# Optimization experiments

Hardware: AMD Instinct MI355X
Metric: run time of the kernel (lower is better)

## Reference

```python
import jax, jax.numpy as jnp
import numpy as np

NUM_ITERS = 3
EPS_ATTN = 1e-8
LN_EPS = 1e-3  # tf.keras LayerNormalization default epsilon


def layernorm(x, g, b):
    m = jnp.mean(x, axis=-1, keepdims=True)
    v = jnp.var(x, axis=-1, keepdims=True)
    return (x - m) * jax.lax.rsqrt(v + LN_EPS) * g + b


def setup_inputs() -> dict:
    key = jax.random.key(0)
    ks = jax.random.split(key, 20)
    B, N, Din, S, D, H = 64, 4096, 64, 7, 64, 128

    def glorot(k, shape):
        fan_in, fan_out = shape[-2], shape[-1]
        lim = np.sqrt(6.0 / (fan_in + fan_out))
        return jax.random.uniform(k, shape, jnp.float32, -lim, lim)

    return {
        "inputs": jax.random.normal(ks[0], (B, N, Din), jnp.float32),
        "slot_noise": jax.random.normal(ks[1], (B, S, D), jnp.float32),
        "ln_in_g": jnp.ones((Din,), jnp.float32), "ln_in_b": jnp.zeros((Din,), jnp.float32),
        "ln_s_g": jnp.ones((D,), jnp.float32), "ln_s_b": jnp.zeros((D,), jnp.float32),
        "ln_m_g": jnp.ones((D,), jnp.float32), "ln_m_b": jnp.zeros((D,), jnp.float32),
        "Wq": glorot(ks[2], (D, D)),
        "Wk": glorot(ks[3], (Din, D)),
        "Wv": glorot(ks[4], (Din, D)),
        "slots_mu": glorot(ks[5], (1, 1, D)),
        "slots_log_sigma": glorot(ks[6], (1, 1, D)),
        "gru_W": glorot(ks[7], (D, 3 * D)),
        "gru_U": glorot(ks[8], (D, 3 * D)),
        "gru_b": jnp.zeros((2, 3 * D), jnp.float32),  # [input_bias, recurrent_bias] (reset_after=True)
        "W1": glorot(ks[9], (D, H)), "b1": jnp.zeros((H,), jnp.float32),
        "W2": glorot(ks[10], (H, D)), "b2": jnp.zeros((D,), jnp.float32),
    }


def reference(inputs, slot_noise, ln_in_g, ln_in_b, ln_s_g, ln_s_b, ln_m_g, ln_m_b,
              Wq, Wk, Wv, slots_mu, slots_log_sigma, gru_W, gru_U, gru_b,
              W1, b1, W2, b2):
    D = Wq.shape[0]
    x = layernorm(inputs, ln_in_g, ln_in_b)          # [B,N,Din]
    k = x @ Wk                                       # [B,N,D]
    v = x @ Wv                                       # [B,N,D]
    slots = slots_mu + jnp.exp(slots_log_sigma) * slot_noise  # [B,S,D]

    scale = D ** (-0.5)
    for _ in range(NUM_ITERS):
        slots_prev = slots
        s = layernorm(slots, ln_s_g, ln_s_b)
        q = (s @ Wq) * scale                         # [B,S,D]
        logits = jnp.einsum("bnd,bsd->bns", k, q)   # [B,N,S]
        attn = jax.nn.softmax(logits, axis=-1) + EPS_ATTN
        attn = attn / jnp.sum(attn, axis=-2, keepdims=True)  # normalize over inputs N
        updates = jnp.einsum("bns,bnd->bsd", attn, v)        # [B,S,D]
        # GRUCell (Keras v2: reset_after=True, sigmoid recurrent activation)
        mx = updates @ gru_W + gru_b[0]
        mh = slots_prev @ gru_U + gru_b[1]
        xz, xr, xh = jnp.split(mx, 3, axis=-1)
        hz, hr, hh = jnp.split(mh, 3, axis=-1)
        z = jax.nn.sigmoid(xz + hz)
        r = jax.nn.sigmoid(xr + hr)
        hcand = jnp.tanh(xh + r * hh)
        slots = z * slots_prev + (1.0 - z) * hcand
        # MLP with residual
        m = layernorm(slots, ln_m_g, ln_m_b)
        slots = slots + jax.nn.relu(m @ W1 + b1) @ W2 + b2
    return slots
```

## Files before the change

### kernel.cpp

```cpp
#include <hip/hip_runtime.h>
#include <hip/hip_bf16.h>


#define NB 64
#define NN 4096
#define NS 7
#define LN_EPS 1e-3f
#define EPS_ATTN 1e-8f

typedef __attribute__((ext_vector_type(8))) __bf16 bf16x8;
typedef __attribute__((ext_vector_type(8))) unsigned short u16x8;
typedef __attribute__((ext_vector_type(4))) float f32x4;
typedef __attribute__((ext_vector_type(4))) unsigned int u32x4;

__device__ __forceinline__ unsigned short f2bf(float f) {
    unsigned int x = __float_as_uint(f);
    x += 0x7FFFu + ((x >> 16) & 1u);
    return (unsigned short)(x >> 16);
}

__device__ __forceinline__ bf16x8 pack8(float4 a, float4 b) {
    u16x8 r;
    r[0] = f2bf(a.x); r[1] = f2bf(a.y); r[2] = f2bf(a.z); r[3] = f2bf(a.w);
    r[4] = f2bf(b.x); r[5] = f2bf(b.y); r[6] = f2bf(b.z); r[7] = f2bf(b.w);
    return __builtin_bit_cast(bf16x8, r);
}

__global__ __launch_bounds__(64) void prep_kernel(
        const float* __restrict__ Wk, const float* __restrict__ Wv,
        const float* __restrict__ g, const float* __restrict__ bb,
        unsigned short* __restrict__ GkT, unsigned short* __restrict__ GvT,
        float* __restrict__ cgk, float* __restrict__ cbk,
        float* __restrict__ cgv, float* __restrict__ cbv) {
    int j = blockIdx.x & 63, mat = blockIdx.x >> 6, d = threadIdx.x;
    const float* W = mat ? Wv : Wk;
    unsigned short* GT = mat ? GvT : GkT;
    float* cg = mat ? cgv : cgk;
    float* cb = mat ? cbv : cbk;
    float w = W[d * 64 + j];
    float gv = g[d], bv = bb[d];
    GT[j * 64 + d] = f2bf(gv * w);
    float sg = gv * w, sb = bv * w;
#pragma unroll
    for (int off = 1; off < 64; off <<= 1) {
        sg += __shfl_xor(sg, off);
        sb += __shfl_xor(sb, off);
    }
    if (d == 0) { cg[j] = sg; cb[j] = sb; }
}

__global__ void init_slots_kernel(const float* __restrict__ noise, const float* __restrict__ mu,
                                  const float* __restrict__ lsig, float* __restrict__ slots) {
    int idx = blockIdx.x * 256 + threadIdx.x;
    if (idx < NB * NS * 64) {
        int d = idx & 63;
        slots[idx] = mu[d] + __expf(lsig[d]) * noise[idx];
    }
}

__global__ __launch_bounds__(256) void proj_kernel(
        const float* __restrict__ x, const unsigned short* __restrict__ GkT,
        const unsigned short* __restrict__ GvT,
        const float* __restrict__ cgk, const float* __restrict__ cbk,
        const float* __restrict__ cgv, const float* __restrict__ cbv,
        unsigned short* __restrict__ kout, unsigned short* __restrict__ vT) {
    int t = threadIdx.x;
    int w = t >> 6, lane = t & 63;
    int h = lane >> 4, rl = lane & 15;
    long base = (long)blockIdx.x * 128;
    int bb = blockIdx.x >> 5;
    int nblk = (blockIdx.x & 31) * 128;
    const float* xr0 = x + (base + w * 16 + rl) * 64 + h * 8;
    const float* xr1 = xr0 + 64 * 64;
    float4 xa[8];
    xa[0] = *(const float4*)(xr0);      xa[1] = *(const float4*)(xr0 + 4);
    xa[2] = *(const float4*)(xr0 + 32); xa[3] = *(const float4*)(xr0 + 36);
    xa[4] = *(const float4*)(xr1);      xa[5] = *(const float4*)(xr1 + 4);
    xa[6] = *(const float4*)(xr1 + 32); xa[7] = *(const float4*)(xr1 + 36);
    float s1a = 0.f, s2a = 0.f, s1b = 0.f, s2b = 0.f;
#pragma unroll
    for (int i = 0; i < 4; ++i) {
        s1a += xa[i].x + xa[i].y + xa[i].z + xa[i].w;
        s2a += xa[i].x * xa[i].x + xa[i].y * xa[i].y + xa[i].z * xa[i].z + xa[i].w * xa[i].w;
        s1b += xa[4 + i].x + xa[4 + i].y + xa[4 + i].z + xa[4 + i].w;
        s2b += xa[4 + i].x * xa[4 + i].x + xa[4 + i].y * xa[4 + i].y + xa[4 + i].z * xa[4 + i].z + xa[4 + i].w * xa[4 + i].w;
    }
    s1a += __shfl_xor(s1a, 16); s2a += __shfl_xor(s2a, 16);
    s1a += __shfl_xor(s1a, 32); s2a += __shfl_xor(s2a, 32);
    s1b += __shfl_xor(s1b, 16); s2b += __shfl_xor(s2b, 16);
    s1b += __shfl_xor(s1b, 32); s2b += __shfl_xor(s2b, 32);
    float m0 = s1a * (1.f / 64.f);
    float i0 = rsqrtf(s2a * (1.f / 64.f) - m0 * m0 + LN_EPS);
    float m1 = s1b * (1.f / 64.f);
    float i1 = rsqrtf(s2b * (1.f / 64.f) - m1 * m1 + LN_EPS);
    bf16x8 a00 = pack8(xa[0], xa[1]), a01 = pack8(xa[2], xa[3]);
    bf16x8 a10 = pack8(xa[4], xa[5]), a11 = pack8(xa[6], xa[7]);
    f32x4 k0a[4], v0a[4], k1a[4], v1a[4];
#pragma unroll
    for (int nt = 0; nt < 4; ++nt) {
        k0a[nt] = (f32x4){0.f, 0.f, 0.f, 0.f}; v0a[nt] = (f32x4){0.f, 0.f, 0.f, 0.f};
        k1a[nt] = (f32x4){0.f, 0.f, 0.f, 0.f}; v1a[nt] = (f32x4){0.f, 0.f, 0.f, 0.f};
    }
#pragma unroll
    for (int nt = 0; nt < 4; ++nt) {
        const unsigned short* gk = GkT + (nt * 16 + rl) * 64 + h * 8;
        const unsigned short* gv = GvT + (nt * 16 + rl) * 64 + h * 8;
        bf16x8 bk0 = *(const bf16x8*)(gk);
        bf16x8 bk1 = *(const bf16x8*)(gk + 32);
        bf16x8 bv0 = *(const bf16x8*)(gv);
        bf16x8 bv1 = *(const bf16x8*)(gv + 32);
        k0a[nt] = __builtin_amdgcn_mfma_f32_16x16x32_bf16(a00, bk0, k0a[nt], 0, 0, 0);
        k0a[nt] = __builtin_amdgcn_mfma_f32_16x16x32_bf16(a01, bk1, k0a[nt], 0, 0, 0);
        v0a[nt] = __builtin_amdgcn_mfma_f32_16x16x32_bf16(a00, bv0, v0a[nt], 0, 0, 0);
        v0a[nt] = __builtin_amdgcn_mfma_f32_16x16x32_bf16(a01, bv1, v0a[nt], 0, 0, 0);
        k1a[nt] = __builtin_amdgcn_mfma_f32_16x16x32_bf16(a10, bk0, k1a[nt], 0, 0, 0);
        k1a[nt] = __builtin_amdgcn_mfma_f32_16x16x32_bf16(a11, bk1, k1a[nt], 0, 0, 0);
        v1a[nt] = __builtin_amdgcn_mfma_f32_16x16x32_bf16(a10, bv0, v1a[nt], 0, 0, 0);
        v1a[nt] = __builtin_amdgcn_mfma_f32_16x16x32_bf16(a11, bv1, v1a[nt], 0, 0, 0);
    }
    float mr0[4], ir0[4], mr1[4], ir1[4];
#pragma unroll
    for (int r = 0; r < 4; ++r) {
        int rlsrc = h * 4 + r;
        mr0[r] = __shfl(m0, rlsrc); ir0[r] = __shfl(i0, rlsrc);
        mr1[r] = __shfl(m1, rlsrc); ir1[r] = __shfl(i1, rlsrc);
    }
#pragma unroll
    for (int nt = 0; nt < 4; ++nt) {
        int j = nt * 16 + rl;
        float cgkj = cgk[j], cbkj = cbk[j], cgvj = cgv[j], cbvj = cbv[j];
        unsigned int vp0 = 0, vp1 = 0;
#pragma unroll
        for (int r = 0; r < 4; ++r) {
            long row = base + w * 16 + h * 4 + r;
            kout[row * 64 + j] = f2bf(ir0[r] * (k0a[nt][r] - mr0[r] * cgkj) + cbkj);
            unsigned int vb = f2bf(ir0[r] * (v0a[nt][r] - mr0[r] * cgvj) + cbvj);
            if (r < 2) vp0 |= vb << (16 * r); else vp1 |= vb << (16 * (r - 2));
        }
        {
            long vaddr = ((long)(bb * 64 + j)) * NN + nblk + w * 16 + h * 4;
            *(uint2*)(vT + vaddr) = make_uint2(vp0, vp1);
        }
        vp0 = 0; vp1 = 0;
#pragma unroll
        for (int r = 0; r < 4; ++r) {
            long row = base + 64 + w * 16 + h * 4 + r;
            kout[row * 64 + j] = f2bf(ir1[r] * (k1a[nt][r] - mr1[r] * cgkj) + cbkj);
            unsigned int vb = f2bf(ir1[r] * (v1a[nt][r] - mr1[r] * cgvj) + cbvj);
            if (r < 2) vp0 |= vb << (16 * r); else vp1 |= vb << (16 * (r - 2));
        }
        {
            long vaddr = ((long)(bb * 64 + j)) * NN + nblk + 64 + w * 16 + h * 4;
            *(uint2*)(vT + vaddr) = make_uint2(vp0, vp1);
        }
    }
}

__global__ __launch_bounds__(64) void slots_pre_kernel(
        const float* __restrict__ slots, const float* __restrict__ Wq,
        const float* __restrict__ lg, const float* __restrict__ lb,
        float* __restrict__ q, float* __restrict__ U, float* __restrict__ Z) {
    __shared__ float sn[64];
    int bs = blockIdx.x, d = threadIdx.x;
    float xv = slots[bs * 64 + d];
    float s1 = xv, s2 = xv * xv;
#pragma unroll
    for (int off = 1; off < 64; off <<= 1) {
        s1 += __shfl_xor(s1, off);
        s2 += __shfl_xor(s2, off);
    }
    float m = s1 * (1.f / 64.f);
    float inv = rsqrtf(s2 * (1.f / 64.f) - m * m + LN_EPS);
    sn[d] = (xv - m) * inv * lg[d] + lb[d];
    __syncthreads();
    float acc = 0.f;
#pragma unroll 8
    for (int i = 0; i < 64; ++i) acc += sn[i] * Wq[i * 64 + d];
    q[bs * 64 + d] = acc * 0.125f;
    U[bs * 64 + d] = 0.f;
    if (d == 0) Z[bs] = 0.f;
}

__global__ __launch_bounds__(256) void attn_kernel(
        const unsigned short* __restrict__ kp, const unsigned short* __restrict__ vtp,
        const float* __restrict__ q, float* __restrict__ U, float* __restrict__ Z) {
    __shared__ unsigned int plds[4][320];
    __shared__ float ured[4][512];
    int t = threadIdx.x;
    int b = blockIdx.x >> 4, blk = blockIdx.x & 15;
    int w = t >> 6, lane = t & 63;
    int h = lane >> 4, c = lane & 15;
    bf16x8 qf0, qf1;
    {
        int cs = (c < 7) ? c : 0;
        const float* qr = q + (b * NS + cs) * 64 + h * 8;
        float4 q0 = *(const float4*)(qr);
        float4 q1 = *(const float4*)(qr + 4);
        float4 q2 = *(const float4*)(qr + 32);
        float4 q3 = *(const float4*)(qr + 36);
        if (c >= 7) {
            q0 = make_float4(0.f, 0.f, 0.f, 0.f); q1 = q0; q2 = q0; q3 = q0;
        }
        qf0 = pack8(q0, q1);
        qf1 = pack8(q2, q3);
    }
    f32x4 pv[4];
#pragma unroll
    for (int i = 0; i < 4; ++i) pv[i] = (f32x4){0.f, 0.f, 0.f, 0.f};
    float zac = 0.f;
    unsigned int* pw = plds[w];
    long rb0 = (long)b * NN + blk * 256 + w * 16;
#pragma unroll
    for (int p = 0; p < 2; ++p) {
#pragma unroll
        for (int sh = 0; sh < 2; ++sh) {
            long rowbase = rb0 + p * 128 + sh * 64;
            const unsigned short* ka = kp + (rowbase + c) * 64 + h * 8;
            bf16x8 a0 = *(const bf16x8*)(ka);
            bf16x8 a1 = *(const bf16x8*)(ka + 32);
            f32x4 lg = (f32x4){0.f, 0.f, 0.f, 0.f};
            lg = __builtin_amdgcn_mfma_f32_16x16x32_bf16(a0, qf0, lg, 0, 0, 0);
            lg = __builtin_amdgcn_mfma_f32_16x16x32_bf16(a1, qf1, lg, 0, 0, 0);
            float av[4];
#pragma unroll
            for (int j = 0; j < 4; ++j) {
                float vl = (c < 7) ? lg[j] : -1e30f;
                float mx = vl;
                mx = fmaxf(mx, __shfl_xor(mx, 1));
                mx = fmaxf(mx, __shfl_xor(mx, 2));
                mx = fmaxf(mx, __shfl_xor(mx, 4));
                mx = fmaxf(mx, __shfl_xor(mx, 8));
                float e = (c < 7) ? __expf(lg[j] - mx) : 0.f;
                float se = e;
                se += __shfl_xor(se, 1);
                se += __shfl_xor(se, 2);
                se += __shfl_xor(se, 4);
                se += __shfl_xor(se, 8);
                float a = (c < 7) ? (__fdividef(e, se) + EPS_ATTN) : 0.f;
                av[j] = a;
                zac += a;
            }
            unsigned int w0 = (unsigned int)f2bf(av[0]) | ((unsigned int)f2bf(av[1]) << 16);
            unsigned int w1 = (unsigned int)f2bf(av[2]) | ((unsigned int)f2bf(av[3]) << 16);
            pw[c * 20 + sh * 8 + 2 * h]     = w0;
            pw[c * 20 + sh * 8 + 2 * h + 1] = w1;
        }
        u32x4 pr = *(u32x4*)(&pw[c * 20 + 4 * h]);
        bf16x8 pa = __builtin_bit_cast(bf16x8, pr);
        int nb = blk * 256 + p * 128 + ((h < 2) ? (w * 16 + 8 * h) : (48 + w * 16 + 8 * h));
#pragma unroll
        for (int tile = 0; tile < 4; ++tile) {
            const unsigned short* vb = vtp + ((long)(b * 64 + tile * 16 + c)) * NN + nb;
            bf16x8 bv = *(const bf16x8*)(vb);
            pv[tile] = __builtin_amdgcn_mfma_f32_16x16x32_bf16(pa, bv, pv[tile], 0, 0, 0);
        }
    }
    zac += __shfl_xor(zac, 16);
    zac += __shfl_xor(zac, 32);
    if (h == 0 && c < 7) atomicAdd(Z + b * NS + c, zac);
    if (h < 2) {
#pragma unroll
        for (int tile = 0; tile < 4; ++tile) {
#pragma unroll
            for (int j = 0; j < 4; ++j) {
                ured[w][(4 * h + j) * 64 + tile * 16 + c] = pv[tile][j];
            }
        }
    }
    __syncthreads();
    for (int idx = t; idx < NS * 64; idx += 256) {
        float tot = ured[0][idx] + ured[1][idx] + ured[2][idx] + ured[3][idx];
        atomicAdd(U + b * NS * 64 + idx, tot);
    }
}

__global__ __launch_bounds__(256) void slots_post_kernel(
        float* __restrict__ slots, float* __restrict__ U, float* __restrict__ Z,
        const float* __restrict__ gW, const float* __restrict__ gU, const float* __restrict__ gb,
        const float* __restrict__ lmg, const float* __restrict__ lmb,
        const float* __restrict__ W1, const float* __restrict__ b1,
        const float* __restrict__ W2, const float* __restrict__ b2,
        const float* __restrict__ Wq, const float* __restrict__ lsg, const float* __restrict__ lsb,
        float* __restrict__ q, float* __restrict__ outp, int last) {
    __shared__ float up[64], hp[64], mx[192], mh[192], mm[64], hl[128], sn[64];
    int bs = blockIdx.x, t = threadIdx.x;
    if (t < 64) {
        float zsum = Z[bs];
        up[t] = U[bs * 64 + t] / zsum;
        hp[t] = slots[bs * 64 + t];
        U[bs * 64 + t] = 0.f;
        if (t == 0) Z[bs] = 0.f;
    }
    __syncthreads();
    if (t < 192) {
        float xa0 = gb[t], ha0 = gb[192 + t], xa1 = 0.f, ha1 = 0.f;
#pragma unroll 8
        for (int i = 0; i < 64; i += 2) {
            xa0 += up[i] * gW[i * 192 + t];
            ha0 += hp[i] * gU[i * 192 + t];
            xa1 += up[i + 1] * gW[(i + 1) * 192 + t];
            ha1 += hp[i + 1] * gU[(i + 1) * 192 + t];
        }
        mx[t] = xa0 + xa1; mh[t] = ha0 + ha1;
    }
    __syncthreads();
    float hnew = 0.f;
    if (t < 64) {
        float z = 1.f / (1.f + __expf(-(mx[t] + mh[t])));
        float r = 1.f / (1.f + __expf(-(mx[64 + t] + mh[64 + t])));
        float pre = mx[128 + t] + r * mh[128 + t];
        pre = fminf(fmaxf(pre, -15.f), 15.f);
        float e2 = __expf(2.f * pre);
        float hc = (e2 - 1.f) / (e2 + 1.f);
        hnew = z * hp[t] + (1.f - z) * hc;
        float s1 = hnew, s2 = hnew * hnew;
#pragma unroll
        for (int off = 1; off < 64; off <<= 1) { s1 += __shfl_xor(s1, off); s2 += __shfl_xor(s2, off); }
        float m = s1 * (1.f / 64.f);
        float inv = rsqrtf(s2 * (1.f / 64.f) - m * m + LN_EPS);
        mm[t] = (hnew - m) * inv * lmg[t] + lmb[t];
    }
    __syncthreads();
    if (t < 128) {
        float h1 = b1[t], h2 = 0.f;
#pragma unroll 8
        for (int i = 0; i < 64; i += 2) {
            h1 += mm[i] * W1[i * 128 + t];
            h2 += mm[i + 1] * W1[(i + 1) * 128 + t];
        }
        hl[t] = fmaxf(h1 + h2, 0.f);
    }
    __syncthreads();
    if (t < 64) {
        float o = hnew + b2[t], o1 = 0.f;
#pragma unroll 8
        for (int j = 0; j < 128; j += 2) {
            o += hl[j] * W2[j * 64 + t];
            o1 += hl[j + 1] * W2[(j + 1) * 64 + t];
        }
        o += o1;
        slots[bs * 64 + t] = o;
        if (last) outp[bs * 64 + t] = o;
        float s1 = o, s2 = o * o;
#pragma unroll
        for (int off = 1; off < 64; off <<= 1) { s1 += __shfl_xor(s1, off); s2 += __shfl_xor(s2, off); }
        float m = s1 * (1.f / 64.f);
        float inv = rsqrtf(s2 * (1.f / 64.f) - m * m + LN_EPS);
        sn[t] = (o - m) * inv * lsg[t] + lsb[t];
    }
    __syncthreads();
    if (t < 64) {
        float acc = 0.f;
#pragma unroll 8
        for (int i = 0; i < 64; ++i) acc += sn[i] * Wq[i * 64 + t];
        q[bs * 64 + t] = acc * 0.125f;
    }
}

extern "C" void kernel_launch(void* const* d_in, const int* in_sizes, int n_in,
                              void* d_out, int out_size, void* d_ws, size_t ws_size,
                              hipStream_t stream) {
    const float* inputs  = (const float*)d_in[0];
    const float* noise   = (const float*)d_in[1];
    const float* ln_in_g = (const float*)d_in[2];
    const float* ln_in_b = (const float*)d_in[3];
    const float* ln_s_g  = (const float*)d_in[4];
    const float* ln_s_b  = (const float*)d_in[5];
    const float* ln_m_g  = (const float*)d_in[6];
    const float* ln_m_b  = (const float*)d_in[7];
    const float* Wq      = (const float*)d_in[8];
    const float* Wk      = (const float*)d_in[9];
    const float* Wv      = (const float*)d_in[10];
    const float* mu      = (const float*)d_in[11];
    const float* lsig    = (const float*)d_in[12];
    const float* gW      = (const float*)d_in[13];
    const float* gU      = (const float*)d_in[14];
    const float* gb      = (const float*)d_in[15];
    const float* W1      = (const float*)d_in[16];
    const float* b1      = (const float*)d_in[17];
    const float* W2      = (const float*)d_in[18];
    const float* b2      = (const float*)d_in[19];

    char* ws = (char*)d_ws;
    unsigned short* kbuf = (unsigned short*)ws;
    unsigned short* vtbuf = (unsigned short*)(ws + 33554432);
    float* slots = (float*)(ws + 67108864);
    float* qbuf  = (float*)(ws + 67108864 + 114688);
    float* Ubuf  = (float*)(ws + 67108864 + 2 * 114688);
    float* Zbuf  = (float*)(ws + 67108864 + 3 * 114688);
    unsigned short* GkT = (unsigned short*)(ws + 67108864 + 3 * 114688 + 4096);
    unsigned short* GvT = GkT + 4096;
    float* cgk = (float*)(GvT + 4096);
    float* cbk = cgk + 64;
    float* cgv = cbk + 64;
    float* cbv = cgv + 64;

    prep_kernel<<<128, 64, 0, stream>>>(Wk, Wv, ln_in_g, ln_in_b, GkT, GvT, cgk, cbk, cgv, cbv);
    init_slots_kernel<<<112, 256, 0, stream>>>(noise, mu, lsig, slots);
    proj_kernel<<<2048, 256, 0, stream>>>(inputs, GkT, GvT, cgk, cbk, cgv, cbv, kbuf, vtbuf);
    slots_pre_kernel<<<448, 64, 0, stream>>>(slots, Wq, ln_s_g, ln_s_b, qbuf, Ubuf, Zbuf);
    for (int it = 0; it < 3; ++it) {
        attn_kernel<<<1024, 256, 0, stream>>>(kbuf, vtbuf, qbuf, Ubuf, Zbuf);
        slots_post_kernel<<<448, 256, 0, stream>>>(slots, Ubuf, Zbuf, gW, gU, gb,
                                                   ln_m_g, ln_m_b, W1, b1, W2, b2,
                                                   Wq, ln_s_g, ln_s_b, qbuf,
                                                   (float*)d_out, (it == 2) ? 1 : 0);
    }
}
```

Before: 256.5 us.

## Stage K/V tiles through LDS for coalesced stores and fuse slot init into projection

The projection kernel now writes its K and transposed V outputs into padded LDS tiles and then emits fully coalesced 16-byte global stores. Slot initialization and the slot pre-processing (layernorm, Q projection, U/Z zeroing) are folded into the first 448 blocks of that kernel, removing two launches. The attention kernel preloads all K fragments into registers and copies its V^T tile into LDS up front instead of issuing scattered global loads inside the loop. The cost is much higher LDS use per block, which may reduce occupancy, plus extra barriers.

Result: no change. 253.1 us (-1.3%).

```diff
diff --git a/kernel.cpp b/kernel.cpp
--- a/kernel.cpp
+++ b/kernel.cpp
@@ -49,21 +49,20 @@
     if (d == 0) { cg[j] = sg; cb[j] = sb; }
 }
 
-__global__ void init_slots_kernel(const float* __restrict__ noise, const float* __restrict__ mu,
-                                  const float* __restrict__ lsig, float* __restrict__ slots) {
-    int idx = blockIdx.x * 256 + threadIdx.x;
-    if (idx < NB * NS * 64) {
-        int d = idx & 63;
-        slots[idx] = mu[d] + __expf(lsig[d]) * noise[idx];
-    }
-}
-
 __global__ __launch_bounds__(256) void proj_kernel(
         const float* __restrict__ x, const unsigned short* __restrict__ GkT,
         const unsigned short* __restrict__ GvT,
         const float* __restrict__ cgk, const float* __restrict__ cbk,
         const float* __restrict__ cgv, const float* __restrict__ cbv,
-        unsigned short* __restrict__ kout, unsigned short* __restrict__ vT) {
+        unsigned short* __restrict__ kout, unsigned short* __restrict__ vT,
+        const float* __restrict__ noise, const float* __restrict__ mu,
+        const float* __restrict__ lsig,
+        const float* __restrict__ Wq, const float* __restrict__ lsg,
+        const float* __restrict__ lsb,
+        float* __restrict__ slots, float* __restrict__ q,
+        float* __restrict__ U, float* __restrict__ Z) {
+    __shared__ __align__(16) unsigned short ktile[128 * 72];
+    __shared__ __align__(16) unsigned short vtile[64 * 136];
     int t = threadIdx.x;
     int w = t >> 6, lane = t & 63;
     int h = lane >> 4, rl = lane & 15;
@@ -83,7 +82,8 @@
         s1a += xa[i].x + xa[i].y + xa[i].z + xa[i].w;
         s2a += xa[i].x * xa[i].x + xa[i].y * xa[i].y + xa[i].z * xa[i].z + xa[i].w * xa[i].w;
         s1b += xa[4 + i].x + xa[4 + i].y + xa[4 + i].z + xa[4 + i].w;
-        s2b += xa[4 + i].x * xa[4 + i].x + xa[4 + i].y * xa[4 + i].y + xa[4 + i].z * xa[4 + i].z + xa[4 + i].w * xa[4 + i].w;
+        s2b += xa[4 + i].x * xa[4 + i].x + xa[4 + i].y * xa[4 + i].y
+             + xa[4 + i].z * xa[4 + i].z + xa[4 + i].w * xa[4 + i].w;
     }
     s1a += __shfl_xor(s1a, 16); s2a += __shfl_xor(s2a, 16);
     s1a += __shfl_xor(s1a, 32); s2a += __shfl_xor(s2a, 32);
@@ -129,67 +129,87 @@
     for (int nt = 0; nt < 4; ++nt) {
         int j = nt * 16 + rl;
         float cgkj = cgk[j], cbkj = cbk[j], cgvj = cgv[j], cbvj = cbv[j];
-        unsigned int vp0 = 0, vp1 = 0;
+        unsigned short vv0[4], vv1[4];
 #pragma unroll
         for (int r = 0; r < 4; ++r) {
-            long row = base + w * 16 + h * 4 + r;
-            kout[row * 64 + j] = f2bf(ir0[r] * (k0a[nt][r] - mr0[r] * cgkj) + cbkj);
-            unsigned int vb = f2bf(ir0[r] * (v0a[nt][r] - mr0[r] * cgvj) + cbvj);
-            if (r < 2) vp0 |= vb << (16 * r); else vp1 |= vb << (16 * (r - 2));
-        }
-        {
-            long vaddr = ((long)(bb * 64 + j)) * NN + nblk + w * 16 + h * 4;
-            *(uint2*)(vT + vaddr) = make_uint2(vp0, vp1);
-        }
-        vp0 = 0; vp1 = 0;
-#pragma unroll
-        for (int r = 0; r < 4; ++r) {
-            long row = base + 64 + w * 16 + h * 4 + r;
-            kout[row * 64 + j] = f2bf(ir1[r] * (k1a[nt][r] - mr1[r] * cgkj) + cbkj);
-            unsigned int vb = f2bf(ir1[r] * (v1a[nt][r] - mr1[r] * cgvj) + cbvj);
-            if (r < 2) vp0 |= vb << (16 * r); else vp1 |= vb << (16 * (r - 2));
-        }
-        {
-            long vaddr = ((long)(bb * 64 + j)) * NN + nblk + 64 + w * 16 + h * 4;
-            *(uint2*)(vT + vaddr) = make_uint2(vp0, vp1);
-        }
-    }
-}
-
-__global__ __launch_bounds__(64) void slots_pre_kernel(
-        const float* __restrict__ slots, const float* __restrict__ Wq,
-        const float* __restrict__ lg, const float* __restrict__ lb,
-        float* __restrict__ q, float* __restrict__ U, float* __restrict__ Z) {
-    __shared__ float sn[64];
-    int bs = blockIdx.x, d = threadIdx.x;
-    float xv = slots[bs * 64 + d];
-    float s1 = xv, s2 = xv * xv;
-#pragma unroll
-    for (int off = 1; off < 64; off <<= 1) {
-        s1 += __shfl_xor(s1, off);
-        s2 += __shfl_xor(s2, off);
-    }
-    float m = s1 * (1.f / 64.f);
-    float inv = rsqrtf(s2 * (1.f / 64.f) - m * m + LN_EPS);
-    sn[d] = (xv - m) * inv * lg[d] + lb[d];
-    __syncthreads();
-    float acc = 0.f;
+            int row = w * 16 + h * 4 + r;
+            ktile[row * 72 + j] = f2bf(ir0[r] * (k0a[nt][r] - mr0[r] * cgkj) + cbkj);
+            ktile[(64 + row) * 72 + j] = f2bf(ir1[r] * (k1a[nt][r] - mr1[r] * cgkj) + cbkj);
+            vv0[r] = f2bf(ir0[r] * (v0a[nt][r] - mr0[r] * cgvj) + cbvj);
+            vv1[r] = f2bf(ir1[r] * (v1a[nt][r] - mr1[r] * cgvj) + cbvj);
+        }
+        uint2 p0 = make_uint2((unsigned int)vv0[0] | ((unsigned int)vv0[1] << 16),
+                              (unsigned int)vv0[2] | ((unsigned int)vv0[3] << 16));
+        uint2 p1 = make_uint2((unsigned int)vv1[0] | ((unsigned int)vv1[1] << 16),
+                              (unsigned int)vv1[2] | ((unsigned int)vv1[3] << 16));
+        *(uint2*)(&vtile[j * 136 + w * 16 + h * 4]) = p0;
+        *(uint2*)(&vtile[j * 136 + 64 + w * 16 + h * 4]) = p1;
+    }
+    __syncthreads();
+#pragma unroll
+    for (int i = 0; i < 4; ++i) {
+        int flat = (i * 256 + t) * 8;
+        int row = flat >> 6, col = flat & 63;
+        uint4 kd = *(const uint4*)(&ktile[row * 72 + col]);
+        *(uint4*)(kout + (base + row) * 64 + col) = kd;
+        int dd = flat >> 7, noff = flat & 127;
+        uint4 vd = *(const uint4*)(&vtile[dd * 136 + noff]);
+        *(uint4*)(vT + ((long)(bb * 64 + dd)) * NN + nblk + noff) = vd;
+    }
+    if (blockIdx.x < 448) {
+        int bs = blockIdx.x;
+        __syncthreads();
+        float* sn = (float*)ktile;
+        if (t < 64) {
+            float xv = mu[t] + __expf(lsig[t]) * noise[bs * 64 + t];
+            slots[bs * 64 + t] = xv;
+            float s1 = xv, s2 = xv * xv;
+#pragma unroll
+            for (int off = 1; off < 64; off <<= 1) {
+                s1 += __shfl_xor(s1, off);
+                s2 += __shfl_xor(s2, off);
+            }
+            float m = s1 * (1.f / 64.f);
+            float inv = rsqrtf(s2 * (1.f / 64.f) - m * m + LN_EPS);
+            sn[t] = (xv - m) * inv * lsg[t] + lsb[t];
+            U[bs * 64 + t] = 0.f;
+            if (t == 0) Z[bs] = 0.f;
+        }
+        __syncthreads();
+        if (t < 64) {
+            float acc = 0.f;
 #pragma unroll 8
-    for (int i = 0; i < 64; ++i) acc += sn[i] * Wq[i * 64 + d];
-    q[bs * 64 + d] = acc * 0.125f;
-    U[bs * 64 + d] = 0.f;
-    if (d == 0) Z[bs] = 0.f;
+            for (int i = 0; i < 64; ++i) acc += sn[i] * Wq[i * 64 + t];
+            q[bs * 64 + t] = acc * 0.125f;
+        }
+    }
 }
 
 __global__ __launch_bounds__(256) void attn_kernel(
         const unsigned short* __restrict__ kp, const unsigned short* __restrict__ vtp,
         const float* __restrict__ q, float* __restrict__ U, float* __restrict__ Z) {
-    __shared__ unsigned int plds[4][320];
-    __shared__ float ured[4][512];
+    __shared__ __align__(16) char smemraw[38912];
+    unsigned short* vtile = (unsigned short*)smemraw;
+    unsigned int* plds = (unsigned int*)(smemraw + 33792);
     int t = threadIdx.x;
     int b = blockIdx.x >> 4, blk = blockIdx.x & 15;
     int w = t >> 6, lane = t & 63;
     int h = lane >> 4, c = lane & 15;
+    long rb0 = (long)b * NN + blk * 256 + w * 16;
+    bf16x8 kf[4][2];
+#pragma unroll
+    for (int i = 0; i < 4; ++i) {
+        const unsigned short* ka = kp + (rb0 + i * 64 + c) * 64 + h * 8;
+        kf[i][0] = *(const bf16x8*)(ka);
+        kf[i][1] = *(const bf16x8*)(ka + 32);
+    }
+#pragma unroll
+    for (int i = 0; i < 8; ++i) {
+        int flat = (i * 256 + t) * 8;
+        int dd = flat >> 8, noff = flat & 255;
+        uint4 vv = *(const uint4*)(vtp + ((long)(b * 64 + dd)) * NN + blk * 256 + noff);
+        *(uint4*)(&vtile[dd * 264 + noff]) = vv;
+    }
     bf16x8 qf0, qf1;
     {
         int cs = (c < 7) ? c : 0;
@@ -208,19 +228,15 @@
 #pragma unroll
     for (int i = 0; i < 4; ++i) pv[i] = (f32x4){0.f, 0.f, 0.f, 0.f};
     float zac = 0.f;
-    unsigned int* pw = plds[w];
-    long rb0 = (long)b * NN + blk * 256 + w * 16;
+    unsigned int* pw = plds + w * 320;
+    __syncthreads();
 #pragma unroll
     for (int p = 0; p < 2; ++p) {
 #pragma unroll
         for (int sh = 0; sh < 2; ++sh) {
-            long rowbase = rb0 + p * 128 + sh * 64;
-            const unsigned short* ka = kp + (rowbase + c) * 64 + h * 8;
-            bf16x8 a0 = *(const bf16x8*)(ka);
-            bf16x8 a1 = *(const bf16x8*)(ka + 32);
             f32x4 lg = (f32x4){0.f, 0.f, 0.f, 0.f};
-            lg = __builtin_amdgcn_mfma_f32_16x16x32_bf16(a0, qf0, lg, 0, 0, 0);
-            lg = __builtin_amdgcn_mfma_f32_16x16x32_bf16(a1, qf1, lg, 0, 0, 0);
+            lg = __builtin_amdgcn_mfma_f32_16x16x32_bf16(kf[p * 2 + sh][0], qf0, lg, 0, 0, 0);
+            lg = __builtin_amdgcn_mfma_f32_16x16x32_bf16(kf[p * 2 + sh][1], qf1, lg, 0, 0, 0);
             float av[4];
 #pragma unroll
             for (int j = 0; j < 4; ++j) {
@@ -247,30 +263,31 @@
         }
         u32x4 pr = *(u32x4*)(&pw[c * 20 + 4 * h]);
         bf16x8 pa = __builtin_bit_cast(bf16x8, pr);
-        int nb = blk * 256 + p * 128 + ((h < 2) ? (w * 16 + 8 * h) : (48 + w * 16 + 8 * h));
+        int nloc = p * 128 + ((h < 2) ? (w * 16 + 8 * h) : (48 + w * 16 + 8 * h));
 #pragma unroll
         for (int tile = 0; tile < 4; ++tile) {
-            const unsigned short* vb = vtp + ((long)(b * 64 + tile * 16 + c)) * NN + nb;
-            bf16x8 bv = *(const bf16x8*)(vb);
+            bf16x8 bv = *(const bf16x8*)(&vtile[(tile * 16 + c) * 264 + nloc]);
             pv[tile] = __builtin_amdgcn_mfma_f32_16x16x32_bf16(pa, bv, pv[tile], 0, 0, 0);
         }
     }
     zac += __shfl_xor(zac, 16);
     zac += __shfl_xor(zac, 32);
     if (h == 0 && c < 7) atomicAdd(Z + b * NS + c, zac);
+    __syncthreads();
+    float* ured = (float*)smemraw;
     if (h < 2) {
 #pragma unroll
         for (int tile = 0; tile < 4; ++tile) {
 #pragma unroll
             for (int j = 0; j < 4; ++j) {
-                ured[w][(4 * h + j) * 64 + tile * 16 + c] = pv[tile][j];
+                ured[w * 512 + (4 * h + j) * 64 + tile * 16 + c] = pv[tile][j];
             }
         }
     }
     __syncthreads();
     for (int idx = t; idx < NS * 64; idx += 256) {
-        float tot = ured[0][idx] + ured[1][idx] + ured[2][idx] + ured[3][idx];
-        atomicAdd(U + b * NS * 64 + idx, tot);
+        float tot = ured[idx] + ured[512 + idx] + ured[1024 + idx] + ured[1536 + idx];
+        atomicAdd(&U[b * (NS * 64) + idx], tot);
     }
 }
 
@@ -382,7 +399,7 @@
     const float* b2      = (const float*)d_in[19];
 
     char* ws = (char*)d_ws;
-    unsigned short* kbuf = (unsigned short*)ws;
+    unsigned short* kbuf  = (unsigned short*)ws;
     unsigned short* vtbuf = (unsigned short*)(ws + 33554432);
     float* slots = (float*)(ws + 67108864);
     float* qbuf  = (float*)(ws + 67108864 + 114688);
@@ -394,16 +411,17 @@
     float* cbk = cgk + 64;
     float* cgv = cbk + 64;
     float* cbv = cgv + 64;
+    float* outp = (float*)d_out;
 
     prep_kernel<<<128, 64, 0, stream>>>(Wk, Wv, ln_in_g, ln_in_b, GkT, GvT, cgk, cbk, cgv, cbv);
-    init_slots_kernel<<<112, 256, 0, stream>>>(noise, mu, lsig, slots);
-    proj_kernel<<<2048, 256, 0, stream>>>(inputs, GkT, GvT, cgk, cbk, cgv, cbv, kbuf, vtbuf);
-    slots_pre_kernel<<<448, 64, 0, stream>>>(slots, Wq, ln_s_g, ln_s_b, qbuf, Ubuf, Zbuf);
+    proj_kernel<<<2048, 256, 0, stream>>>(inputs, GkT, GvT, cgk, cbk, cgv, cbv, kbuf, vtbuf,
+                                          noise, mu, lsig, Wq, ln_s_g, ln_s_b,
+                                          slots, qbuf, Ubuf, Zbuf);
     for (int it = 0; it < 3; ++it) {
         attn_kernel<<<1024, 256, 0, stream>>>(kbuf, vtbuf, qbuf, Ubuf, Zbuf);
         slots_post_kernel<<<448, 256, 0, stream>>>(slots, Ubuf, Zbuf, gW, gU, gb,
                                                    ln_m_g, ln_m_b, W1, b1, W2, b2,
                                                    Wq, ln_s_g, ln_s_b, qbuf,
-                                                   (float*)d_out, (it == 2) ? 1 : 0);
-    }
-}
+                                                   outp, (it == 2) ? 1 : 0);
+    }
+}
```
